# Kernel optimization log

Measured on AMD Instinct MI355X. Metric: run time of the kernel, lower is better.

## Reference

```python
import jax, jax.numpy as jnp
import numpy as np

B, N, M, D = 64, 197, 65, 768


def setup_inputs() -> dict:
    key = jax.random.key(0)
    k1, k2, k3 = jax.random.split(key, 3)
    image = jax.random.normal(k1, (B, N, D), dtype=jnp.float32)
    text = jax.random.normal(k2, (B, M, D), dtype=jnp.float32)
    pm = jax.random.randint(k3, (B, M), 0, 2).astype(jnp.int32)
    pm = pm.at[:, :2].set(0)  # CLS + first real token always valid
    logit_scale = jnp.ones((), dtype=jnp.float32)
    return {"image": image, "text": text, "padding_masks": pm, "logit_scale": logit_scale}


def _ce_with_diag_labels(logits):
    # F.cross_entropy(logits, arange(B)): mean of -log_softmax diag
    return -jnp.mean(jnp.diagonal(jax.nn.log_softmax(logits, axis=-1)))


def reference(image, text, padding_masks, logit_scale):
    # include_cls_token=False: original computes full [B,B,N,M] then slices
    # [:, :, 1:, 1:]; we compute the sliced tokens directly (same math).
    img = image[:, 1:, :]                   # [B, N-1, D]
    txt = text[:, 1:, :]                    # [B, M-1, D]
    pm = padding_masks[:, 1:].astype(bool)  # [B, M-1] True = padded

    # sim[i,j,n,m] = logit_scale * <img_i,n , txt_j,m>
    sim = logit_scale * jnp.einsum('ind,jmd->ijnm', img, txt)  # [B,B,N-1,M-1]

    # Original masks with NaN along mask of batch-row i (broadcast over j,n).
    # logits_per_image: nan_to_num(-inf) -> max over m -> mean over n
    sim_img = jnp.where(pm[:, None, None, :], -jnp.inf, sim)
    logits_per_image = jnp.mean(jnp.max(sim_img, axis=3), axis=2)  # [B,B]

    # logits_per_text: max over n (NaN cols stay NaN) -> nanmean over m.
    # Equivalent masked mean over valid m (mask constant along n).
    max_n = jnp.max(sim, axis=2)                         # [B,B,M-1]
    valid = ~pm                                          # [B,M-1]
    cnt = jnp.sum(valid, axis=1).astype(sim.dtype)       # [B]
    logits_per_text = jnp.sum(
        jnp.where(valid[:, None, :], max_n, 0.0), axis=2
    ) / cnt[:, None]                                     # [B,B]

    loss = 0.5 * (_ce_with_diag_labels(logits_per_image)
                  + _ce_with_diag_labels(logits_per_text))
    targets = jnp.arange(logits_per_image.shape[0], dtype=jnp.int32)
    return loss, logits_per_image, logits_per_text, targets
```

## Files before the change

### kernel.cpp

```cpp
#include <hip/hip_runtime.h>

typedef _Float16 half8 __attribute__((ext_vector_type(8)));
typedef float floatx4 __attribute__((ext_vector_type(4)));
typedef float float4v __attribute__((ext_vector_type(4)));

#define DIM   768
#define NROW  196
#define AUNITS (64 * 13 * 24 * 64)
#define TUNITS (64 * 4 * 24 * 64)
#define A_HALFS ((size_t)AUNITS * 8)
#define BJ_HALFS (24 * 4 * 64 * 8)

__device__ __forceinline__ void gl_lds16(const _Float16* g, _Float16* l) {
  __builtin_amdgcn_global_load_lds(
      (const __attribute__((address_space(1))) unsigned int*)g,
      (__attribute__((address_space(3))) unsigned int*)l, 16, 0, 0);
}

__global__ __launch_bounds__(256) void repack(const float* __restrict__ img,
                                              const float* __restrict__ txt,
                                              _Float16* __restrict__ Apk,
                                              _Float16* __restrict__ Bpk) {
  int gid = blockIdx.x * 256 + threadIdx.x;
  const float* src;
  _Float16* dst;
  if (gid < AUNITS) {
    int l = gid & 63, g = gid >> 6;
    int s = g % 24; g /= 24;
    int tau = g % 13; int i = g / 13;
    int n = tau * 16 + (l & 15); if (n > 195) n = 195;
    src = img + (size_t)i * 197 * 768 + (size_t)(n + 1) * 768 + s * 32 + (l >> 4) * 8;
    dst = Apk + (size_t)gid * 8;
  } else {
    int u = gid - AUNITS;
    int l = u & 63, g = u >> 6;
    int ct = g & 3; g >>= 2;
    int s = g % 24; int j = g / 24;
    int m = ct * 16 + (l & 15);
    src = txt + (size_t)j * 65 * 768 + (size_t)(m + 1) * 768 + s * 32 + (l >> 4) * 8;
    dst = Bpk + (size_t)u * 8;
  }
  float4v v0 = *(const float4v*)src;
  float4v v1 = *(const float4v*)(src + 4);
  half8 h;
  h[0] = (_Float16)v0[0]; h[1] = (_Float16)v0[1]; h[2] = (_Float16)v0[2]; h[3] = (_Float16)v0[3];
  h[4] = (_Float16)v1[0]; h[5] = (_Float16)v1[1]; h[6] = (_Float16)v1[2]; h[7] = (_Float16)v1[3];
  *(half8*)dst = h;
}

__global__ __launch_bounds__(256, 3) void sim_kernel(const _Float16* __restrict__ Apk,
                                                     const _Float16* __restrict__ Bpk,
                                                     const int* __restrict__ pm,
                                                     const float* __restrict__ ls,
                                                     float* __restrict__ lpi,
                                                     float* __restrict__ lpt) {
  __shared__ _Float16 Bsh[8192];

  const int j = blockIdx.x, i = blockIdx.y;
  const int tid = threadIdx.x;
  const int wave = tid >> 6, lane = tid & 63;
  const int r16 = lane & 15;
  const int lane8 = lane * 8;

  const _Float16* Ai = Apk + (size_t)i * 13 * 24 * 512;
  const _Float16* pA[4];
  pA[0] = Ai + (size_t)(wave)     * 24 * 512 + lane8;
  pA[1] = Ai + (size_t)(wave + 4) * 24 * 512 + lane8;
  pA[2] = Ai + (size_t)(wave + 8) * 24 * 512 + lane8;
  pA[3] = Ai + (size_t)12         * 24 * 512 + lane8;
  const _Float16* Bg = Bpk + (size_t)j * BJ_HALFS;

#pragma unroll
  for (int r2 = 0; r2 < 2; ++r2) {
    int rr = wave * 2 + r2;
    gl_lds16(Bg + rr * 512 + lane8, Bsh + rr * 512);
  }

  half8 af[2][4];
#pragma unroll
  for (int d = 0; d < 2; ++d)
#pragma unroll
    for (int t = 0; t < 4; ++t)
      af[d][t] = *(const half8*)(pA[t] + d * 512);

  floatx4 acc[3][4];
  floatx4 acc12 = (floatx4){0.f, 0.f, 0.f, 0.f};
#pragma unroll
  for (int t = 0; t < 3; ++t)
#pragma unroll
    for (int cc = 0; cc < 4; ++cc)
      acc[t][cc] = (floatx4){0.f, 0.f, 0.f, 0.f};

#pragma unroll
  for (int c = 0; c < 12; ++c) {
    __syncthreads();
    if (c < 11) {
#pragma unroll
      for (int r2 = 0; r2 < 2; ++r2) {
        int rr = wave * 2 + r2;
        gl_lds16(Bg + (c + 1) * 4096 + rr * 512 + lane8,
                 Bsh + ((c + 1) & 1) * 4096 + rr * 512);
      }
    }
#pragma unroll
    for (int sc = 0; sc < 2; ++sc) {
      const int s = c * 2 + sc;
      const int base = (c & 1) * 4096 + sc * 2048 + lane8;
      half8 b0[4];
#pragma unroll
      for (int cc = 0; cc < 4; ++cc) {
        int ct = (wave + cc) & 3;
        b0[cc] = *(const half8*)(Bsh + base + ct * 512);
      }
      half8 a0 = af[s & 1][0], a1 = af[s & 1][1], a2 = af[s & 1][2], a3 = af[s & 1][3];
      if (s < 22) {
#pragma unroll
        for (int t = 0; t < 4; ++t) af[s & 1][t] = *(const half8*)(pA[t] + (s + 2) * 512);
      }
#pragma unroll
      for (int cc = 0; cc < 4; ++cc) {
        acc[0][cc] = __builtin_amdgcn_mfma_f32_16x16x32_f16(a0, b0[cc], acc[0][cc], 0, 0, 0);
        acc[1][cc] = __builtin_amdgcn_mfma_f32_16x16x32_f16(a1, b0[cc], acc[1][cc], 0, 0, 0);
        acc[2][cc] = __builtin_amdgcn_mfma_f32_16x16x32_f16(a2, b0[cc], acc[2][cc], 0, 0, 0);
      }
      acc12 = __builtin_amdgcn_mfma_f32_16x16x32_f16(a3, b0[0], acc12, 0, 0, 0);
    }
  }

  const float sgl = ls[0];
  bool msk[4];
  int colc[4];
#pragma unroll
  for (int cc = 0; cc < 4; ++cc) {
    colc[cc] = ((wave + cc) & 3) * 16 + r16;
    msk[cc] = pm[i * 65 + 1 + colc[cc]] != 0;
  }

  float rowsum = 0.f;
  float cmv[4];
#pragma unroll
  for (int t = 0; t < 3; ++t) {
#pragma unroll
    for (int r = 0; r < 4; ++r) {
      float rm = -__builtin_inff();
#pragma unroll
      for (int cc = 0; cc < 4; ++cc) {
        float v = acc[t][cc][r] * sgl;
        rm = fmaxf(rm, msk[cc] ? -__builtin_inff() : v);
      }
#pragma unroll
      for (int off = 1; off < 16; off <<= 1)
        rm = fmaxf(rm, __shfl_xor(rm, off, 64));
      rowsum += rm;
    }
  }
#pragma unroll
  for (int off = 1; off < 64; off <<= 1) rowsum += __shfl_xor(rowsum, off, 64);

#pragma unroll
  for (int cc = 0; cc < 4; ++cc) {
    float cm = -__builtin_inff();
#pragma unroll
    for (int t = 0; t < 3; ++t)
#pragma unroll
      for (int r = 0; r < 4; ++r)
        cm = fmaxf(cm, acc[t][cc][r] * sgl);
    cm = fmaxf(cm, __shfl_xor(cm, 16, 64));
    cm = fmaxf(cm, __shfl_xor(cm, 32, 64));
    cmv[cc] = cm;
  }

  __syncthreads();
  float* colmaxS = (float*)Bsh;
  float* t12S    = (float*)Bsh + 256;
  float* wsumS   = (float*)Bsh + 512;

  if (lane == 0) wsumS[wave] = rowsum;
  if (lane < 16) {
#pragma unroll
    for (int cc = 0; cc < 4; ++cc) colmaxS[wave * 64 + colc[cc]] = cmv[cc];
#pragma unroll
    for (int r = 0; r < 4; ++r) t12S[r * 64 + wave * 16 + r16] = acc12[r] * sgl;
  }
  __syncthreads();

  if (tid < 64) {
    const int col = lane;
    bool valid = pm[i * 65 + 1 + col] == 0;
    float t0 = t12S[col], t1 = t12S[64 + col], t2 = t12S[128 + col], t3 = t12S[192 + col];
    float v = fmaxf(fmaxf(colmaxS[col], colmaxS[64 + col]),
                    fmaxf(colmaxS[128 + col], colmaxS[192 + col]));
    v = fmaxf(v, fmaxf(fmaxf(t0, t1), fmaxf(t2, t3)));
    float contrib = valid ? v : 0.f;
    float cntv = valid ? 1.f : 0.f;
    float rs0 = valid ? t0 : -__builtin_inff();
    float rs1 = valid ? t1 : -__builtin_inff();
    float rs2 = valid ? t2 : -__builtin_inff();
    float rs3 = valid ? t3 : -__builtin_inff();
#pragma unroll
    for (int off = 1; off < 64; off <<= 1) {
      contrib += __shfl_xor(contrib, off, 64);
      cntv += __shfl_xor(cntv, off, 64);
      rs0 = fmaxf(rs0, __shfl_xor(rs0, off, 64));
      rs1 = fmaxf(rs1, __shfl_xor(rs1, off, 64));
      rs2 = fmaxf(rs2, __shfl_xor(rs2, off, 64));
      rs3 = fmaxf(rs3, __shfl_xor(rs3, off, 64));
    }
    if (lane == 0) {
      lpt[i * 64 + j] = contrib / cntv;
      float wtot = wsumS[0] + wsumS[1] + wsumS[2] + wsumS[3];
      lpi[i * 64 + j] = (wtot * 0.0625f + rs0 + rs1 + rs2 + rs3) / 196.f;
    }
  }
}

__global__ __launch_bounds__(64) void ce_kernel(float* __restrict__ out) {
  const int t = threadIdx.x;
  const float* lpi = out + 1;
  const float* lpt = out + 1 + 4096;

  float mx = -__builtin_inff();
#pragma unroll
  for (int jj = 0; jj < 64; ++jj) mx = fmaxf(mx, lpi[t * 64 + jj]);
  float se = 0.f;
#pragma unroll
  for (int jj = 0; jj < 64; ++jj) se += __expf(lpi[t * 64 + jj] - mx);
  float ci = (mx + __logf(se)) - lpi[t * 64 + t];

  float mx2 = -__builtin_inff();
#pragma unroll
  for (int jj = 0; jj < 64; ++jj) mx2 = fmaxf(mx2, lpt[t * 64 + jj]);
  float se2 = 0.f;
#pragma unroll
  for (int jj = 0; jj < 64; ++jj) se2 += __expf(lpt[t * 64 + jj] - mx2);
  float ct_ = (mx2 + __logf(se2)) - lpt[t * 64 + t];

  float v = ci + ct_;
#pragma unroll
  for (int off = 1; off < 64; off <<= 1) v += __shfl_xor(v, off, 64);
  if (t == 0) out[0] = 0.5f * v / 64.f;
  out[1 + 8192 + t] = (float)t;
}

extern "C" void kernel_launch(void* const* d_in, const int* in_sizes, int n_in,
                              void* d_out, int out_size, void* d_ws, size_t ws_size,
                              hipStream_t stream) {
  const float* image = (const float*)d_in[0];
  const float* text  = (const float*)d_in[1];
  const int*   pm    = (const int*)d_in[2];
  const float* ls    = (const float*)d_in[3];
  float* out = (float*)d_out;

  _Float16* Apk = (_Float16*)d_ws;
  _Float16* Bpk = Apk + A_HALFS;

  repack<<<(AUNITS + TUNITS) / 256, 256, 0, stream>>>(image, text, Apk, Bpk);

  dim3 grid(64, 64);
  sim_kernel<<<grid, 256, 0, stream>>>(Apk, Bpk, pm, ls, out + 1, out + 1 + 4096);
  ce_kernel<<<1, 64, 0, stream>>>(out);
}
```

Measured before the change: 194.8 us.

## Process two text batches per block with 512 threads and deeper B staging

Measured after the change: 346.6 us. 1.78x slower.

```diff
diff --git a/kernel.cpp b/kernel.cpp
--- a/kernel.cpp
+++ b/kernel.cpp
@@ -48,33 +48,37 @@
   *(half8*)dst = h;
 }
 
-__global__ __launch_bounds__(256, 3) void sim_kernel(const _Float16* __restrict__ Apk,
+__global__ __launch_bounds__(512, 4) void sim_kernel(const _Float16* __restrict__ Apk,
                                                      const _Float16* __restrict__ Bpk,
                                                      const int* __restrict__ pm,
                                                      const float* __restrict__ ls,
                                                      float* __restrict__ lpi,
                                                      float* __restrict__ lpt) {
-  __shared__ _Float16 Bsh[8192];
-
-  const int j = blockIdx.x, i = blockIdx.y;
+  __shared__ _Float16 Bsh[32768];
+
+  const int jb = blockIdx.x, i = blockIdx.y;
   const int tid = threadIdx.x;
   const int wave = tid >> 6, lane = tid & 63;
+  const int w4 = wave & 3, jj = wave >> 2;
   const int r16 = lane & 15;
   const int lane8 = lane * 8;
 
   const _Float16* Ai = Apk + (size_t)i * 13 * 24 * 512;
   const _Float16* pA[4];
-  pA[0] = Ai + (size_t)(wave)     * 24 * 512 + lane8;
-  pA[1] = Ai + (size_t)(wave + 4) * 24 * 512 + lane8;
-  pA[2] = Ai + (size_t)(wave + 8) * 24 * 512 + lane8;
-  pA[3] = Ai + (size_t)12         * 24 * 512 + lane8;
-  const _Float16* Bg = Bpk + (size_t)j * BJ_HALFS;
-
-#pragma unroll
-  for (int r2 = 0; r2 < 2; ++r2) {
-    int rr = wave * 2 + r2;
-    gl_lds16(Bg + rr * 512 + lane8, Bsh + rr * 512);
-  }
+  pA[0] = Ai + (size_t)(w4)     * 24 * 512 + lane8;
+  pA[1] = Ai + (size_t)(w4 + 4) * 24 * 512 + lane8;
+  pA[2] = Ai + (size_t)(w4 + 8) * 24 * 512 + lane8;
+  pA[3] = Ai + (size_t)12       * 24 * 512 + lane8;
+  const _Float16* Bg = Bpk + (size_t)(2 * jb) * BJ_HALFS;
+
+#pragma unroll
+  for (int r4 = 0; r4 < 4; ++r4) {
+    int u = wave * 4 + r4;
+    int jjd = u >> 4, rr = u & 15;
+    gl_lds16(Bg + (size_t)jjd * BJ_HALFS + rr * 512 + lane8,
+             Bsh + jjd * 8192 + rr * 512);
+  }
+  __builtin_amdgcn_sched_barrier(0);
 
   half8 af[2][4];
 #pragma unroll
@@ -92,38 +96,54 @@
       acc[t][cc] = (floatx4){0.f, 0.f, 0.f, 0.f};
 
 #pragma unroll
-  for (int c = 0; c < 12; ++c) {
-    __syncthreads();
-    if (c < 11) {
-#pragma unroll
-      for (int r2 = 0; r2 < 2; ++r2) {
-        int rr = wave * 2 + r2;
-        gl_lds16(Bg + (c + 1) * 4096 + rr * 512 + lane8,
-                 Bsh + ((c + 1) & 1) * 4096 + rr * 512);
-      }
-    }
-#pragma unroll
-    for (int sc = 0; sc < 2; ++sc) {
-      const int s = c * 2 + sc;
-      const int base = (c & 1) * 4096 + sc * 2048 + lane8;
-      half8 b0[4];
+  for (int c = 0; c < 6; ++c) {
+#pragma unroll
+    for (int sc = 0; sc < 4; ++sc) {
+      const int s = c * 4 + sc;
+
+      if (sc == 0) {
+        if (c == 0) asm volatile("s_waitcnt vmcnt(8)" ::: "memory");
+        else        asm volatile("s_waitcnt vmcnt(12)" ::: "memory");
+        __builtin_amdgcn_s_barrier();
+        __builtin_amdgcn_sched_barrier(0);
+      }
+
+      const int base = (c & 1) * 16384 + jj * 8192 + sc * 2048 + lane8;
+      half8 b[4];
 #pragma unroll
       for (int cc = 0; cc < 4; ++cc) {
-        int ct = (wave + cc) & 3;
-        b0[cc] = *(const half8*)(Bsh + base + ct * 512);
-      }
+        int ct = (w4 + cc) & 3;
+        b[cc] = *(const half8*)(Bsh + base + ct * 512);
+      }
+
+      if (c < 5 && sc < 2) {
+#pragma unroll
+        for (int r2 = 0; r2 < 2; ++r2) {
+          int u = wave * 4 + sc * 2 + r2;
+          int jjd = u >> 4, rr = u & 15;
+          gl_lds16(Bg + (size_t)jjd * BJ_HALFS + (c + 1) * 8192 + rr * 512 + lane8,
+                   Bsh + ((c + 1) & 1) * 16384 + jjd * 8192 + rr * 512);
+        }
+        if (sc == 1) __builtin_amdgcn_sched_barrier(0);
+      }
+
       half8 a0 = af[s & 1][0], a1 = af[s & 1][1], a2 = af[s & 1][2], a3 = af[s & 1][3];
       if (s < 22) {
 #pragma unroll
         for (int t = 0; t < 4; ++t) af[s & 1][t] = *(const half8*)(pA[t] + (s + 2) * 512);
       }
+
+      __builtin_amdgcn_s_barrier();
+
+      __builtin_amdgcn_s_setprio(1);
 #pragma unroll
       for (int cc = 0; cc < 4; ++cc) {
-        acc[0][cc] = __builtin_amdgcn_mfma_f32_16x16x32_f16(a0, b0[cc], acc[0][cc], 0, 0, 0);
-        acc[1][cc] = __builtin_amdgcn_mfma_f32_16x16x32_f16(a1, b0[cc], acc[1][cc], 0, 0, 0);
-        acc[2][cc] = __builtin_amdgcn_mfma_f32_16x16x32_f16(a2, b0[cc], acc[2][cc], 0, 0, 0);
-      }
-      acc12 = __builtin_amdgcn_mfma_f32_16x16x32_f16(a3, b0[0], acc12, 0, 0, 0);
+        acc[0][cc] = __builtin_amdgcn_mfma_f32_16x16x32_f16(a0, b[cc], acc[0][cc], 0, 0, 0);
+        acc[1][cc] = __builtin_amdgcn_mfma_f32_16x16x32_f16(a1, b[cc], acc[1][cc], 0, 0, 0);
+        acc[2][cc] = __builtin_amdgcn_mfma_f32_16x16x32_f16(a2, b[cc], acc[2][cc], 0, 0, 0);
+      }
+      acc12 = __builtin_amdgcn_mfma_f32_16x16x32_f16(a3, b[0], acc12, 0, 0, 0);
+      __builtin_amdgcn_s_setprio(0);
     }
   }
 
@@ -132,7 +152,7 @@
   int colc[4];
 #pragma unroll
   for (int cc = 0; cc < 4; ++cc) {
-    colc[cc] = ((wave + cc) & 3) * 16 + r16;
+    colc[cc] = ((w4 + cc) & 3) * 16 + r16;
     msk[cc] = pm[i * 65 + 1 + colc[cc]] != 0;
   }
 
@@ -172,24 +192,26 @@
 
   __syncthreads();
   float* colmaxS = (float*)Bsh;
-  float* t12S    = (float*)Bsh + 256;
-  float* wsumS   = (float*)Bsh + 512;
-
-  if (lane == 0) wsumS[wave] = rowsum;
+  float* t12S    = (float*)Bsh + 512;
+  float* wsumS   = (float*)Bsh + 1024;
+
+  if (lane == 0) wsumS[jj * 4 + w4] = rowsum;
   if (lane < 16) {
 #pragma unroll
-    for (int cc = 0; cc < 4; ++cc) colmaxS[wave * 64 + colc[cc]] = cmv[cc];
-#pragma unroll
-    for (int r = 0; r < 4; ++r) t12S[r * 64 + wave * 16 + r16] = acc12[r] * sgl;
+    for (int cc = 0; cc < 4; ++cc) colmaxS[jj * 256 + w4 * 64 + colc[cc]] = cmv[cc];
+#pragma unroll
+    for (int r = 0; r < 4; ++r) t12S[jj * 256 + r * 64 + w4 * 16 + r16] = acc12[r] * sgl;
   }
   __syncthreads();
 
-  if (tid < 64) {
+  if (tid < 128) {
+    const int jjf = wave;
     const int col = lane;
     bool valid = pm[i * 65 + 1 + col] == 0;
-    float t0 = t12S[col], t1 = t12S[64 + col], t2 = t12S[128 + col], t3 = t12S[192 + col];
-    float v = fmaxf(fmaxf(colmaxS[col], colmaxS[64 + col]),
-                    fmaxf(colmaxS[128 + col], colmaxS[192 + col]));
+    const float* cm = colmaxS + jjf * 256;
+    const float* t12 = t12S + jjf * 256;
+    float t0 = t12[col], t1 = t12[64 + col], t2 = t12[128 + col], t3 = t12[192 + col];
+    float v = fmaxf(fmaxf(cm[col], cm[64 + col]), fmaxf(cm[128 + col], cm[192 + col]));
     v = fmaxf(v, fmaxf(fmaxf(t0, t1), fmaxf(t2, t3)));
     float contrib = valid ? v : 0.f;
     float cntv = valid ? 1.f : 0.f;
@@ -207,9 +229,10 @@
       rs3 = fmaxf(rs3, __shfl_xor(rs3, off, 64));
     }
     if (lane == 0) {
-      lpt[i * 64 + j] = contrib / cntv;
-      float wtot = wsumS[0] + wsumS[1] + wsumS[2] + wsumS[3];
-      lpi[i * 64 + j] = (wtot * 0.0625f + rs0 + rs1 + rs2 + rs3) / 196.f;
+      int jout = 2 * jb + jjf;
+      lpt[i * 64 + jout] = contrib / cntv;
+      float wtot = wsumS[jjf * 4 + 0] + wsumS[jjf * 4 + 1] + wsumS[jjf * 4 + 2] + wsumS[jjf * 4 + 3];
+      lpi[i * 64 + jout] = (wtot * 0.0625f + rs0 + rs1 + rs2 + rs3) / 196.f;
     }
   }
 }
@@ -256,7 +279,7 @@
 
   repack<<<(AUNITS + TUNITS) / 256, 256, 0, stream>>>(image, text, Apk, Bpk);
 
-  dim3 grid(64, 64);
-  sim_kernel<<<grid, 256, 0, stream>>>(Apk, Bpk, pm, ls, out + 1, out + 1 + 4096);
+  dim3 grid(32, 64);
+  sim_kernel<<<grid, 512, 0, stream>>>(Apk, Bpk, pm, ls, out + 1, out + 1 + 4096);
   ce_kernel<<<1, 64, 0, stream>>>(out);
 }
```

## Stage A and B tiles in LDS and compute four j per 512-thread block

Applied to the files above, without the earlier changes.

New measurement: 181.8 us. -6.7%, faster.

```diff
diff --git a/kernel.cpp b/kernel.cpp
--- a/kernel.cpp
+++ b/kernel.cpp
@@ -4,12 +4,11 @@
 typedef float floatx4 __attribute__((ext_vector_type(4)));
 typedef float float4v __attribute__((ext_vector_type(4)));
 
-#define DIM   768
-#define NROW  196
 #define AUNITS (64 * 13 * 24 * 64)
 #define TUNITS (64 * 4 * 24 * 64)
 #define A_HALFS ((size_t)AUNITS * 8)
 #define BJ_HALFS (24 * 4 * 64 * 8)
+#define AI_HALFS (13 * 24 * 512)
 
 __device__ __forceinline__ void gl_lds16(const _Float16* g, _Float16* l) {
   __builtin_amdgcn_global_load_lds(
@@ -48,168 +47,161 @@
   *(half8*)dst = h;
 }
 
-__global__ __launch_bounds__(256, 3) void sim_kernel(const _Float16* __restrict__ Apk,
+__global__ __launch_bounds__(512, 2) void sim_kernel(const _Float16* __restrict__ Apk,
                                                      const _Float16* __restrict__ Bpk,
                                                      const int* __restrict__ pm,
                                                      const float* __restrict__ ls,
                                                      float* __restrict__ lpi,
                                                      float* __restrict__ lpt) {
-  __shared__ _Float16 Bsh[8192];
-
-  const int j = blockIdx.x, i = blockIdx.y;
+  __shared__ _Float16 Lds[59392];
+
+  const int jb4 = blockIdx.x, i = blockIdx.y;
   const int tid = threadIdx.x;
   const int wave = tid >> 6, lane = tid & 63;
+  const int wr = wave >> 2, wc = wave & 3;
+  const int NT = 7 - wr;
   const int r16 = lane & 15;
   const int lane8 = lane * 8;
 
-  const _Float16* Ai = Apk + (size_t)i * 13 * 24 * 512;
-  const _Float16* pA[4];
-  pA[0] = Ai + (size_t)(wave)     * 24 * 512 + lane8;
-  pA[1] = Ai + (size_t)(wave + 4) * 24 * 512 + lane8;
-  pA[2] = Ai + (size_t)(wave + 8) * 24 * 512 + lane8;
-  pA[3] = Ai + (size_t)12         * 24 * 512 + lane8;
-  const _Float16* Bg = Bpk + (size_t)j * BJ_HALFS;
-
-#pragma unroll
-  for (int r2 = 0; r2 < 2; ++r2) {
-    int rr = wave * 2 + r2;
-    gl_lds16(Bg + rr * 512 + lane8, Bsh + rr * 512);
-  }
-
-  half8 af[2][4];
-#pragma unroll
-  for (int d = 0; d < 2; ++d)
-#pragma unroll
-    for (int t = 0; t < 4; ++t)
-      af[d][t] = *(const half8*)(pA[t] + d * 512);
-
-  floatx4 acc[3][4];
-  floatx4 acc12 = (floatx4){0.f, 0.f, 0.f, 0.f};
-#pragma unroll
-  for (int t = 0; t < 3; ++t)
-#pragma unroll
-    for (int cc = 0; cc < 4; ++cc)
-      acc[t][cc] = (floatx4){0.f, 0.f, 0.f, 0.f};
+  _Float16* LB = Lds;
+  _Float16* LA = Lds + 32768;
+  const _Float16* Ag = Apk + (size_t)i * AI_HALFS;
+  const _Float16* Bg = Bpk + (size_t)(4 * jb4) * BJ_HALFS + (size_t)(wave & 3) * BJ_HALFS;
+
+  auto stage = [&](int cc) {
+    const int buf = cc & 1;
+    if (wave < 4) {
+#pragma unroll
+      for (int k = 0; k < 8; ++k) {
+        int sc = k >> 2, ct = k & 3;
+        gl_lds16(Bg + (size_t)(2 * cc + sc) * 2048 + ct * 512 + lane8,
+                 LB + buf * 16384 + wave * 4096 + sc * 2048 + ct * 512);
+      }
+    } else {
+#pragma unroll
+      for (int k = 0; k < 8; ++k) {
+        int m = (wave - 4) * 8 + k;
+        int tau = m >> 1; if (tau > 12) tau = 12;
+        int sc = m & 1;
+        gl_lds16(Ag + (size_t)tau * 12288 + (size_t)(2 * cc + sc) * 512 + lane8,
+                 LA + buf * 13312 + sc * 6656 + tau * 512);
+      }
+    }
+  };
+
+  stage(0);
+
+  floatx4 acc[7][4];
+#pragma unroll
+  for (int t = 0; t < 7; ++t)
+#pragma unroll
+    for (int n = 0; n < 4; ++n)
+      acc[t][n] = (floatx4){0.f, 0.f, 0.f, 0.f};
 
 #pragma unroll
   for (int c = 0; c < 12; ++c) {
-    __syncthreads();
-    if (c < 11) {
-#pragma unroll
-      for (int r2 = 0; r2 < 2; ++r2) {
-        int rr = wave * 2 + r2;
-        gl_lds16(Bg + (c + 1) * 4096 + rr * 512 + lane8,
-                 Bsh + ((c + 1) & 1) * 4096 + rr * 512);
-      }
-    }
+    asm volatile("s_waitcnt vmcnt(0)" ::: "memory");
+    __builtin_amdgcn_s_barrier();
+    __builtin_amdgcn_sched_barrier(0);
+    if (c < 11) stage(c + 1);
+
 #pragma unroll
     for (int sc = 0; sc < 2; ++sc) {
-      const int s = c * 2 + sc;
-      const int base = (c & 1) * 4096 + sc * 2048 + lane8;
-      half8 b0[4];
-#pragma unroll
-      for (int cc = 0; cc < 4; ++cc) {
-        int ct = (wave + cc) & 3;
-        b0[cc] = *(const half8*)(Bsh + base + ct * 512);
-      }
-      half8 a0 = af[s & 1][0], a1 = af[s & 1][1], a2 = af[s & 1][2], a3 = af[s & 1][3];
-      if (s < 22) {
-#pragma unroll
-        for (int t = 0; t < 4; ++t) af[s & 1][t] = *(const half8*)(pA[t] + (s + 2) * 512);
-      }
-#pragma unroll
-      for (int cc = 0; cc < 4; ++cc) {
-        acc[0][cc] = __builtin_amdgcn_mfma_f32_16x16x32_f16(a0, b0[cc], acc[0][cc], 0, 0, 0);
-        acc[1][cc] = __builtin_amdgcn_mfma_f32_16x16x32_f16(a1, b0[cc], acc[1][cc], 0, 0, 0);
-        acc[2][cc] = __builtin_amdgcn_mfma_f32_16x16x32_f16(a2, b0[cc], acc[2][cc], 0, 0, 0);
-      }
-      acc12 = __builtin_amdgcn_mfma_f32_16x16x32_f16(a3, b0[0], acc12, 0, 0, 0);
+      half8 b[4];
+#pragma unroll
+      for (int n = 0; n < 4; ++n) {
+        int ct = (n + 2 * wr) & 3;
+        b[n] = *(const half8*)(LB + (c & 1) * 16384 + wc * 4096 + sc * 2048 + ct * 512 + lane8);
+      }
+      half8 a[7];
+#pragma unroll
+      for (int t = 0; t < 7; ++t)
+        if (t < NT)
+          a[t] = *(const half8*)(LA + (c & 1) * 13312 + sc * 6656 + (wr * 7 + t) * 512 + lane8);
+
+      __builtin_amdgcn_s_setprio(1);
+#pragma unroll
+      for (int t = 0; t < 7; ++t)
+        if (t < NT) {
+#pragma unroll
+          for (int n = 0; n < 4; ++n)
+            acc[t][n] = __builtin_amdgcn_mfma_f32_16x16x32_f16(a[t], b[n], acc[t][n], 0, 0, 0);
+        }
+      __builtin_amdgcn_s_setprio(0);
     }
   }
 
   const float sgl = ls[0];
-  bool msk[4];
-  int colc[4];
-#pragma unroll
-  for (int cc = 0; cc < 4; ++cc) {
-    colc[cc] = ((wave + cc) & 3) * 16 + r16;
-    msk[cc] = pm[i * 65 + 1 + colc[cc]] != 0;
+  int colc[4]; bool msk[4];
+#pragma unroll
+  for (int n = 0; n < 4; ++n) {
+    colc[n] = ((n + 2 * wr) & 3) * 16 + r16;
+    msk[n] = pm[i * 65 + 1 + colc[n]] != 0;
   }
 
   float rowsum = 0.f;
-  float cmv[4];
-#pragma unroll
-  for (int t = 0; t < 3; ++t) {
-#pragma unroll
-    for (int r = 0; r < 4; ++r) {
-      float rm = -__builtin_inff();
-#pragma unroll
-      for (int cc = 0; cc < 4; ++cc) {
-        float v = acc[t][cc][r] * sgl;
-        rm = fmaxf(rm, msk[cc] ? -__builtin_inff() : v);
-      }
-#pragma unroll
-      for (int off = 1; off < 16; off <<= 1)
-        rm = fmaxf(rm, __shfl_xor(rm, off, 64));
-      rowsum += rm;
-    }
-  }
+#pragma unroll
+  for (int t = 0; t < 7; ++t)
+    if (t < NT) {
+#pragma unroll
+      for (int r = 0; r < 4; ++r) {
+        float rm = -__builtin_inff();
+#pragma unroll
+        for (int n = 0; n < 4; ++n) {
+          float v = acc[t][n][r] * sgl;
+          rm = fmaxf(rm, msk[n] ? -__builtin_inff() : v);
+        }
+#pragma unroll
+        for (int off = 1; off < 16; off <<= 1)
+          rm = fmaxf(rm, __shfl_xor(rm, off, 64));
+        bool vrow = (wr == 0) || (t < 5) || ((lane >> 4) == 0);
+        rowsum += vrow ? rm : 0.f;
+      }
+    }
 #pragma unroll
   for (int off = 1; off < 64; off <<= 1) rowsum += __shfl_xor(rowsum, off, 64);
 
-#pragma unroll
-  for (int cc = 0; cc < 4; ++cc) {
-    float cm = -__builtin_inff();
-#pragma unroll
-    for (int t = 0; t < 3; ++t)
-#pragma unroll
-      for (int r = 0; r < 4; ++r)
-        cm = fmaxf(cm, acc[t][cc][r] * sgl);
-    cm = fmaxf(cm, __shfl_xor(cm, 16, 64));
-    cm = fmaxf(cm, __shfl_xor(cm, 32, 64));
-    cmv[cc] = cm;
+  float cm[4];
+#pragma unroll
+  for (int n = 0; n < 4; ++n) {
+    float c = -__builtin_inff();
+#pragma unroll
+    for (int t = 0; t < 7; ++t)
+      if (t < NT) {
+#pragma unroll
+        for (int r = 0; r < 4; ++r) c = fmaxf(c, acc[t][n][r] * sgl);
+      }
+    c = fmaxf(c, __shfl_xor(c, 16, 64));
+    c = fmaxf(c, __shfl_xor(c, 32, 64));
+    cm[n] = c;
   }
 
   __syncthreads();
-  float* colmaxS = (float*)Bsh;
-  float* t12S    = (float*)Bsh + 256;
-  float* wsumS   = (float*)Bsh + 512;
-
-  if (lane == 0) wsumS[wave] = rowsum;
+  float* colmaxS = (float*)Lds;
+  float* wsumS   = (float*)Lds + 512;
+
   if (lane < 16) {
 #pragma unroll
-    for (int cc = 0; cc < 4; ++cc) colmaxS[wave * 64 + colc[cc]] = cmv[cc];
-#pragma unroll
-    for (int r = 0; r < 4; ++r) t12S[r * 64 + wave * 16 + r16] = acc12[r] * sgl;
-  }
+    for (int n = 0; n < 4; ++n) colmaxS[(wc * 2 + wr) * 64 + colc[n]] = cm[n];
+  }
+  if (lane == 0) wsumS[wc * 2 + wr] = rowsum;
   __syncthreads();
 
-  if (tid < 64) {
-    const int col = lane;
+  if (tid < 256) {
+    const int j = wave, col = lane;
     bool valid = pm[i * 65 + 1 + col] == 0;
-    float t0 = t12S[col], t1 = t12S[64 + col], t2 = t12S[128 + col], t3 = t12S[192 + col];
-    float v = fmaxf(fmaxf(colmaxS[col], colmaxS[64 + col]),
-                    fmaxf(colmaxS[128 + col], colmaxS[192 + col]));
-    v = fmaxf(v, fmaxf(fmaxf(t0, t1), fmaxf(t2, t3)));
+    float v = fmaxf(colmaxS[(j * 2 + 0) * 64 + col], colmaxS[(j * 2 + 1) * 64 + col]);
     float contrib = valid ? v : 0.f;
     float cntv = valid ? 1.f : 0.f;
-    float rs0 = valid ? t0 : -__builtin_inff();
-    float rs1 = valid ? t1 : -__builtin_inff();
-    float rs2 = valid ? t2 : -__builtin_inff();
-    float rs3 = valid ? t3 : -__builtin_inff();
 #pragma unroll
     for (int off = 1; off < 64; off <<= 1) {
       contrib += __shfl_xor(contrib, off, 64);
       cntv += __shfl_xor(cntv, off, 64);
-      rs0 = fmaxf(rs0, __shfl_xor(rs0, off, 64));
-      rs1 = fmaxf(rs1, __shfl_xor(rs1, off, 64));
-      rs2 = fmaxf(rs2, __shfl_xor(rs2, off, 64));
-      rs3 = fmaxf(rs3, __shfl_xor(rs3, off, 64));
     }
     if (lane == 0) {
-      lpt[i * 64 + j] = contrib / cntv;
-      float wtot = wsumS[0] + wsumS[1] + wsumS[2] + wsumS[3];
-      lpi[i * 64 + j] = (wtot * 0.0625f + rs0 + rs1 + rs2 + rs3) / 196.f;
+      int jout = 4 * jb4 + j;
+      lpt[i * 64 + jout] = contrib / cntv;
+      lpi[i * 64 + jout] = (wsumS[j * 2] + wsumS[j * 2 + 1]) * 0.0625f / 196.f;
     }
   }
 }
@@ -256,7 +248,7 @@
 
   repack<<<(AUNITS + TUNITS) / 256, 256, 0, stream>>>(image, text, Apk, Bpk);
 
-  dim3 grid(64, 64);
-  sim_kernel<<<grid, 256, 0, stream>>>(Apk, Bpk, pm, ls, out + 1, out + 1 + 4096);
+  dim3 grid(16, 64);
+  sim_kernel<<<grid, 512, 0, stream>>>(Apk, Bpk, pm, ls, out + 1, out + 1 + 4096);
   ce_kernel<<<1, 64, 0, stream>>>(out);
 }
```

## Restage sim_kernel B pipeline into larger double-buffered chunks with explicit waitcnt

Applied to the files above, without the earlier changes.

After: 184.0 us. 5.6% less time.

```diff
diff --git a/kernel.cpp b/kernel.cpp
--- a/kernel.cpp
+++ b/kernel.cpp
@@ -4,12 +4,11 @@
 typedef float floatx4 __attribute__((ext_vector_type(4)));
 typedef float float4v __attribute__((ext_vector_type(4)));
 
-#define DIM   768
-#define NROW  196
 #define AUNITS (64 * 13 * 24 * 64)
 #define TUNITS (64 * 4 * 24 * 64)
 #define A_HALFS ((size_t)AUNITS * 8)
 #define BJ_HALFS (24 * 4 * 64 * 8)
+#define AI_HALFS (13 * 24 * 512)
 
 __device__ __forceinline__ void gl_lds16(const _Float16* g, _Float16* l) {
   __builtin_amdgcn_global_load_lds(
@@ -48,13 +47,13 @@
   *(half8*)dst = h;
 }
 
-__global__ __launch_bounds__(256, 3) void sim_kernel(const _Float16* __restrict__ Apk,
+__global__ __launch_bounds__(256, 4) void sim_kernel(const _Float16* __restrict__ Apk,
                                                      const _Float16* __restrict__ Bpk,
                                                      const int* __restrict__ pm,
                                                      const float* __restrict__ ls,
                                                      float* __restrict__ lpi,
                                                      float* __restrict__ lpt) {
-  __shared__ _Float16 Bsh[8192];
+  __shared__ _Float16 Bsh[16384];
 
   const int j = blockIdx.x, i = blockIdx.y;
   const int tid = threadIdx.x;
@@ -62,7 +61,7 @@
   const int r16 = lane & 15;
   const int lane8 = lane * 8;
 
-  const _Float16* Ai = Apk + (size_t)i * 13 * 24 * 512;
+  const _Float16* Ai = Apk + (size_t)i * AI_HALFS;
   const _Float16* pA[4];
   pA[0] = Ai + (size_t)(wave)     * 24 * 512 + lane8;
   pA[1] = Ai + (size_t)(wave + 4) * 24 * 512 + lane8;
@@ -70,18 +69,25 @@
   pA[3] = Ai + (size_t)12         * 24 * 512 + lane8;
   const _Float16* Bg = Bpk + (size_t)j * BJ_HALFS;
 
-#pragma unroll
-  for (int r2 = 0; r2 < 2; ++r2) {
-    int rr = wave * 2 + r2;
-    gl_lds16(Bg + rr * 512 + lane8, Bsh + rr * 512);
-  }
-
-  half8 af[2][4];
-#pragma unroll
-  for (int d = 0; d < 2; ++d)
-#pragma unroll
-    for (int t = 0; t < 4; ++t)
-      af[d][t] = *(const half8*)(pA[t] + d * 512);
+  auto stage = [&](int cc) {
+    const int buf = cc & 1;
+#pragma unroll
+    for (int r4 = 0; r4 < 4; ++r4) {
+      int rr = wave * 4 + r4;
+      gl_lds16(Bg + (size_t)(4 * cc) * 2048 + rr * 512 + lane8,
+               Bsh + buf * 8192 + rr * 512);
+    }
+  };
+
+  stage(0);
+  __builtin_amdgcn_sched_barrier(0);
+  half8 af[4];
+#pragma unroll
+  for (int t = 0; t < 4; ++t) af[t] = *(const half8*)(pA[t]);
+  __builtin_amdgcn_sched_barrier(0);
+  asm volatile("s_waitcnt vmcnt(4)" ::: "memory");
+  __builtin_amdgcn_s_barrier();
+  __builtin_amdgcn_sched_barrier(0);
 
   floatx4 acc[3][4];
   floatx4 acc12 = (floatx4){0.f, 0.f, 0.f, 0.f};
@@ -92,38 +98,45 @@
       acc[t][cc] = (floatx4){0.f, 0.f, 0.f, 0.f};
 
 #pragma unroll
-  for (int c = 0; c < 12; ++c) {
-    __syncthreads();
-    if (c < 11) {
-#pragma unroll
-      for (int r2 = 0; r2 < 2; ++r2) {
-        int rr = wave * 2 + r2;
-        gl_lds16(Bg + (c + 1) * 4096 + rr * 512 + lane8,
-                 Bsh + ((c + 1) & 1) * 4096 + rr * 512);
-      }
-    }
-#pragma unroll
-    for (int sc = 0; sc < 2; ++sc) {
-      const int s = c * 2 + sc;
-      const int base = (c & 1) * 4096 + sc * 2048 + lane8;
-      half8 b0[4];
+  for (int c = 0; c < 6; ++c) {
+#pragma unroll
+    for (int sc = 0; sc < 4; ++sc) {
+      const int s = c * 4 + sc;
+
+      if (sc == 0 && c > 0) {
+        asm volatile("s_waitcnt vmcnt(16)" ::: "memory");
+        __builtin_amdgcn_s_barrier();
+        __builtin_amdgcn_sched_barrier(0);
+      }
+
+      const int base = (c & 1) * 8192 + sc * 2048 + lane8;
+      half8 b[4];
 #pragma unroll
       for (int cc = 0; cc < 4; ++cc) {
         int ct = (wave + cc) & 3;
-        b0[cc] = *(const half8*)(Bsh + base + ct * 512);
-      }
-      half8 a0 = af[s & 1][0], a1 = af[s & 1][1], a2 = af[s & 1][2], a3 = af[s & 1][3];
-      if (s < 22) {
-#pragma unroll
-        for (int t = 0; t < 4; ++t) af[s & 1][t] = *(const half8*)(pA[t] + (s + 2) * 512);
-      }
+        b[cc] = *(const half8*)(Bsh + base + ct * 512);
+      }
+
+      if (sc == 0 && c < 5) {
+        stage(c + 1);
+        __builtin_amdgcn_sched_barrier(0);
+      }
+
+      __builtin_amdgcn_s_setprio(1);
 #pragma unroll
       for (int cc = 0; cc < 4; ++cc) {
-        acc[0][cc] = __builtin_amdgcn_mfma_f32_16x16x32_f16(a0, b0[cc], acc[0][cc], 0, 0, 0);
-        acc[1][cc] = __builtin_amdgcn_mfma_f32_16x16x32_f16(a1, b0[cc], acc[1][cc], 0, 0, 0);
-        acc[2][cc] = __builtin_amdgcn_mfma_f32_16x16x32_f16(a2, b0[cc], acc[2][cc], 0, 0, 0);
-      }
-      acc12 = __builtin_amdgcn_mfma_f32_16x16x32_f16(a3, b0[0], acc12, 0, 0, 0);
+        acc[0][cc] = __builtin_amdgcn_mfma_f32_16x16x32_f16(af[0], b[cc], acc[0][cc], 0, 0, 0);
+        acc[1][cc] = __builtin_amdgcn_mfma_f32_16x16x32_f16(af[1], b[cc], acc[1][cc], 0, 0, 0);
+        acc[2][cc] = __builtin_amdgcn_mfma_f32_16x16x32_f16(af[2], b[cc], acc[2][cc], 0, 0, 0);
+      }
+      acc12 = __builtin_amdgcn_mfma_f32_16x16x32_f16(af[3], b[0], acc12, 0, 0, 0);
+      __builtin_amdgcn_s_setprio(0);
+
+      if (s < 23) {
+#pragma unroll
+        for (int t = 0; t < 4; ++t) af[t] = *(const half8*)(pA[t] + (s + 1) * 512);
+      }
+      __builtin_amdgcn_sched_barrier(0);
     }
   }
 
@@ -214,32 +227,26 @@
   }
 }
 
-__global__ __launch_bounds__(64) void ce_kernel(float* __restrict__ out) {
-  const int t = threadIdx.x;
-  const float* lpi = out + 1;
-  const float* lpt = out + 1 + 4096;
+__global__ __launch_bounds__(128) void ce_kernel(float* __restrict__ out) {
+  __shared__ float part[2];
+  const int tid = threadIdx.x;
+  const int t = tid & 63;
+  const float* src = (tid < 64) ? (out + 1) : (out + 1 + 4096);
 
   float mx = -__builtin_inff();
 #pragma unroll
-  for (int jj = 0; jj < 64; ++jj) mx = fmaxf(mx, lpi[t * 64 + jj]);
+  for (int jj = 0; jj < 64; ++jj) mx = fmaxf(mx, src[t * 64 + jj]);
   float se = 0.f;
 #pragma unroll
-  for (int jj = 0; jj < 64; ++jj) se += __expf(lpi[t * 64 + jj] - mx);
-  float ci = (mx + __logf(se)) - lpi[t * 64 + t];
-
-  float mx2 = -__builtin_inff();
-#pragma unroll
-  for (int jj = 0; jj < 64; ++jj) mx2 = fmaxf(mx2, lpt[t * 64 + jj]);
-  float se2 = 0.f;
-#pragma unroll
-  for (int jj = 0; jj < 64; ++jj) se2 += __expf(lpt[t * 64 + jj] - mx2);
-  float ct_ = (mx2 + __logf(se2)) - lpt[t * 64 + t];
-
-  float v = ci + ct_;
+  for (int jj = 0; jj < 64; ++jj) se += __expf(src[t * 64 + jj] - mx);
+  float v = (mx + __logf(se)) - src[t * 64 + t];
+
 #pragma unroll
   for (int off = 1; off < 64; off <<= 1) v += __shfl_xor(v, off, 64);
-  if (t == 0) out[0] = 0.5f * v / 64.f;
-  out[1 + 8192 + t] = (float)t;
+  if (t == 0) part[tid >> 6] = v;
+  __syncthreads();
+  if (tid == 0) out[0] = 0.5f * (part[0] + part[1]) / 64.f;
+  if (tid < 64) out[1 + 8192 + tid] = (float)tid;
 }
 
 extern "C" void kernel_launch(void* const* d_in, const int* in_sizes, int n_in,
@@ -258,5 +265,5 @@
 
   dim3 grid(64, 64);
   sim_kernel<<<grid, 256, 0, stream>>>(Apk, Bpk, pm, ls, out + 1, out + 1 + 4096);
-  ce_kernel<<<1, 64, 0, stream>>>(out);
-}
+  ce_kernel<<<1, 128, 0, stream>>>(out);
+}
```
